# Kernel tuning notes

Hardware: AMD Instinct MI355X
Metric: run time of the kernel (lower is better)

The kernel has to match this reference:

```python
import jax, jax.numpy as jnp
import numpy as np

B, F, D, A = 1024, 33, 128, 128  # batch, num_fields, embed_dim, attn_size (A must equal gnn dim)

def setup_inputs() -> dict:
    key = jax.random.key(0)
    k1, k2, k3, k4 = jax.random.split(key, 4)
    gnn_feature = jax.random.normal(k1, (B, A), dtype=jnp.float32)
    x = jax.random.normal(k2, (B, F, D), dtype=jnp.float32)
    # attention Linear(embed_dim -> attn_size): weight (A, D), bias (A,)
    lim = 1.0 / np.sqrt(D)
    attn_W = jax.random.uniform(k3, (A, D), minval=-lim, maxval=lim, dtype=jnp.float32)
    attn_b = jax.random.uniform(k4, (A,), minval=-lim, maxval=lim, dtype=jnp.float32)
    return {"gnn_feature": gnn_feature, "x": x, "attn_W": attn_W, "attn_b": attn_b}

def reference(gnn_feature, x, attn_W, attn_b):
    num_fields = x.shape[1]
    row, col = np.triu_indices(num_fields, k=1)  # P = F*(F-1)/2 pairs
    inner = x[:, row] * x[:, col]                # [B, P, D]
    fm = jax.nn.relu(jnp.einsum('bpd,ad->bpa', inner, attn_W) + attn_b)  # [B, P, A]
    # bmm(gnn[b,1,A], fm[b,p,A,1]) -> dot product per pair, softmax over pairs
    scores = jnp.einsum('ba,bpa->bp', gnn_feature, fm)  # [B, P]
    attn = jax.nn.softmax(scores, axis=1)               # [B, P]
    attn_output = jnp.einsum('bp,bpd->bd', attn, inner) * 100.0  # [B, D]
    return jnp.concatenate([gnn_feature, attn_output], axis=1)   # [B, A+D]
```

## Files before the change

kernel.cpp:

```cpp
#include <hip/hip_runtime.h>

#define FN 33
#define DN 128
#define AN 128
#define PN 528
#define MTN 33
#define XS 136
#define AS 36

typedef __attribute__((ext_vector_type(8))) _Float16 half8;
typedef __attribute__((ext_vector_type(2))) _Float16 h2;
typedef __attribute__((ext_vector_type(4))) float f32x4;
typedef __attribute__((ext_vector_type(2))) float f32x2;
typedef __attribute__((ext_vector_type(4))) unsigned int u32x4;

__device__ __forceinline__ unsigned int pkrtz(float a, float b) {
  return __builtin_bit_cast(unsigned int, __builtin_amdgcn_cvt_pkrtz(a, b));
}
__device__ __forceinline__ h2 ash2(unsigned int u) { return __builtin_bit_cast(h2, u); }

__device__ __forceinline__ float row_sum16(float v) {
  v += __builtin_bit_cast(float, __builtin_amdgcn_update_dpp(0, __builtin_bit_cast(int, v), 0x128, 0xF, 0xF, false));
  v += __builtin_bit_cast(float, __builtin_amdgcn_update_dpp(0, __builtin_bit_cast(int, v), 0x124, 0xF, 0xF, false));
  v += __builtin_bit_cast(float, __builtin_amdgcn_update_dpp(0, __builtin_bit_cast(int, v), 0x122, 0xF, 0xF, false));
  v += __builtin_bit_cast(float, __builtin_amdgcn_update_dpp(0, __builtin_bit_cast(int, v), 0x121, 0xF, 0xF, false));
  return v;
}

__global__ __launch_bounds__(256, 2)
void afm_kernel(const float* __restrict__ gnn, const float* __restrict__ xg,
                const float* __restrict__ Wg,  const float* __restrict__ bg,
                float* __restrict__ out)
{
  __shared__ __align__(16) _Float16 xh[FN * XS];
  __shared__ __align__(16) unsigned int attn_h2[FN * AS];
  __shared__ __align__(16) float scores_s[PN];
  __shared__ __align__(16) float part[512];
  __shared__ unsigned short rowcol[PN];
  __shared__ float red[8];

  const int tid  = threadIdx.x;
  const int wave = tid >> 6;
  const int lane = tid & 63;
  const int q    = lane >> 4;
  const int u    = lane & 15;

  for (int p = tid; p < PN; p += 256) {
    int i = 0, rem = p;
    while (rem >= FN - 1 - i) { rem -= FN - 1 - i; i++; }
    rowcol[p] = (unsigned short)(i | ((i + 1 + rem) << 8));
  }
  half8 Bf[8][4];
  #pragma unroll
  for (int n = 0; n < 8; n++) {
    const float* wrow = Wg + (size_t)(n * 16 + u) * DN + q * 8;
    #pragma unroll
    for (int kk = 0; kk < 4; kk++) {
      f32x4 w0 = *(const f32x4*)(wrow + kk * 32);
      f32x4 w1 = *(const f32x4*)(wrow + kk * 32 + 4);
      union { half8 h; unsigned int w[4]; } t;
      t.w[0] = pkrtz(w0.x, w0.y);
      t.w[1] = pkrtz(w0.z, w0.w);
      t.w[2] = pkrtz(w1.x, w1.y);
      t.w[3] = pkrtz(w1.z, w1.w);
      Bf[n][kk] = t.h;
      asm volatile("" : "+v"(Bf[n][kk]));
    }
  }
  float barr[8];
  #pragma unroll
  for (int n = 0; n < 8; n++) { barr[n] = bg[n * 16 + u]; asm volatile("" : "+v"(barr[n])); }

  #pragma unroll 1
  for (int r2 = 0; r2 < 2; r2++) {
    const int b = blockIdx.x * 2 + r2;

    float garr[8];
    #pragma unroll
    for (int n = 0; n < 8; n++) { garr[n] = gnn[(size_t)b * AN + n * 16 + u]; asm volatile("" : "+v"(garr[n])); }

    const f32x4* xg4 = (const f32x4*)(xg + (size_t)b * FN * DN);
    for (int idx = tid; idx < (FN * DN) / 4; idx += 256) {
      f32x4 v = xg4[idx];
      int i  = idx >> 5;
      int d0 = (idx & 31) << 2;
      *(uint2*)&xh[i * XS + d0] = make_uint2(pkrtz(v.x, v.y), pkrtz(v.z, v.w));
    }
    for (int idx = tid; idx < FN * AS; idx += 256) attn_h2[idx] = 0u;
    __syncthreads();

    {
      int mt = wave;
      unsigned int rc = rowcol[mt * 16 + u];
      int r = rc & 255, c = rc >> 8;
      half8 xr[4], xc[4];
      #pragma unroll
      for (int kk = 0; kk < 4; kk++) {
        xr[kk] = *(const half8*)&xh[r * XS + kk * 32 + q * 8];
        xc[kk] = *(const half8*)&xh[c * XS + kk * 32 + q * 8];
      }
      for (;;) {
        half8 Af[4];
        #pragma unroll
        for (int kk = 0; kk < 4; kk++) Af[kk] = xr[kk] * xc[kk];

        const int nmt = mt + 4;
        if (nmt < MTN) {
          rc = rowcol[nmt * 16 + u];
          r = rc & 255; c = rc >> 8;
          #pragma unroll
          for (int kk = 0; kk < 4; kk++) {
            xr[kk] = *(const half8*)&xh[r * XS + kk * 32 + q * 8];
            xc[kk] = *(const half8*)&xh[c * XS + kk * 32 + q * 8];
          }
        }

        float sc[4] = {0.f, 0.f, 0.f, 0.f};
        #pragma unroll
        for (int g = 0; g < 2; g++) {
          f32x4 acc[4];
          #pragma unroll
          for (int nn = 0; nn < 4; nn++) {
            float bv = barr[g * 4 + nn];
            acc[nn] = (f32x4){bv, bv, bv, bv};
          }
          #pragma unroll
          for (int kk = 0; kk < 4; kk++)
            #pragma unroll
            for (int nn = 0; nn < 4; nn++)
              acc[nn] = __builtin_amdgcn_mfma_f32_16x16x32_f16(Af[kk], Bf[g * 4 + nn][kk], acc[nn], 0, 0, 0);
          #pragma unroll
          for (int nn = 0; nn < 4; nn++)
            #pragma unroll
            for (int rr = 0; rr < 4; rr++) {
              float fmv = fmaxf(acc[nn][rr], 0.f);
              sc[rr] = fmaf(fmv, garr[g * 4 + nn], sc[rr]);
            }
        }
        #pragma unroll
        for (int rr = 0; rr < 4; rr++) sc[rr] = row_sum16(sc[rr]);
        if (u == 0)
          *(f32x4*)&scores_s[mt * 16 + q * 4] = (f32x4){sc[0], sc[1], sc[2], sc[3]};

        if (nmt >= MTN) break;
        mt = nmt;
      }
    }
    __syncthreads();

    float s0 = scores_s[tid];
    float s1 = scores_s[tid + 256];
    float s2 = (tid < 16) ? scores_s[tid + 512] : -3.4e38f;
    float m = fmaxf(fmaxf(s0, s1), s2);
    #pragma unroll
    for (int off = 32; off >= 1; off >>= 1) m = fmaxf(m, __shfl_xor(m, off, 64));
    if (lane == 0) red[wave] = m;
    __syncthreads();
    const float smax = fmaxf(fmaxf(red[0], red[1]), fmaxf(red[2], red[3]));

    float e0 = __expf(s0 - smax);
    float e1 = __expf(s1 - smax);
    float e2 = (tid < 16) ? __expf(s2 - smax) : 0.f;
    {
      unsigned int rc = rowcol[tid];
      attn_h2[(rc & 255) * AS + ((rc >> 8) - (rc & 255) - 1)] = pkrtz(e0, e0);
      rc = rowcol[tid + 256];
      attn_h2[(rc & 255) * AS + ((rc >> 8) - (rc & 255) - 1)] = pkrtz(e1, e1);
      if (tid < 16) {
        rc = rowcol[tid + 512];
        attn_h2[(rc & 255) * AS + ((rc >> 8) - (rc & 255) - 1)] = pkrtz(e2, e2);
      }
    }
    float lsum = e0 + e1 + e2;
    #pragma unroll
    for (int off = 32; off >= 1; off >>= 1) lsum += __shfl_xor(lsum, off, 64);
    if (lane == 0) red[4 + wave] = lsum;
    __syncthreads();
    const float Z = red[4] + red[5] + red[6] + red[7];

    {
      unsigned int xp[36];
      #pragma unroll
      for (int j = 0; j < FN; j++) xp[j] = *(const unsigned int*)&xh[j * XS + 2 * lane];
      xp[33] = 0u; xp[34] = 0u; xp[35] = 0u;

      float a0 = 0.f, a1 = 0.f;
      #pragma unroll
      for (int i = 0; i < 32; i++) {
        if ((i & 3) != wave) continue;
        const int L   = 32 - i;
        const int n4  = (L + 3) >> 2;
        h2 ti2 = (h2)0.0f;
        #pragma unroll
        for (int t = 0; t < 8; t++) {
          if (t >= n4) break;
          u32x4 a4 = *(const u32x4*)&attn_h2[i * AS + 4 * t];
          ti2 += ash2(a4.x) * ash2(xp[i + 1 + 4 * t + 0]);
          ti2 += ash2(a4.y) * ash2(xp[i + 1 + 4 * t + 1]);
          ti2 += ash2(a4.z) * ash2(xp[i + 1 + 4 * t + 2]);
          ti2 += ash2(a4.w) * ash2(xp[i + 1 + 4 * t + 3]);
        }
        h2 xi = ash2(xp[i]);
        a0 = fmaf((float)xi[0], (float)ti2[0], a0);
        a1 = fmaf((float)xi[1], (float)ti2[1], a1);
      }
      *(f32x2*)&part[wave * 128 + 2 * lane] = (f32x2){a0, a1};
    }
    __syncthreads();
    if (tid < DN) {
      float tot = (part[tid] + part[128 + tid]) + (part[256 + tid] + part[384 + tid]);
      out[(size_t)b * (AN + DN) + AN + tid] = tot * (100.0f / Z);
    } else {
      const int a = tid - 128;
      out[(size_t)b * (AN + DN) + a] = gnn[(size_t)b * AN + a];
    }
  }
}

extern "C" void kernel_launch(void* const* d_in, const int* in_sizes, int n_in,
                              void* d_out, int out_size, void* d_ws, size_t ws_size,
                              hipStream_t stream) {
  (void)n_in; (void)out_size; (void)d_ws; (void)ws_size;
  const float* gnn  = (const float*)d_in[0];
  const float* x    = (const float*)d_in[1];
  const float* W    = (const float*)d_in[2];
  const float* bias = (const float*)d_in[3];
  float* out = (float*)d_out;
  const int Bn = in_sizes[0] / AN;
  afm_kernel<<<dim3(Bn / 2), dim3(256), 0, stream>>>(gnn, x, W, bias, out);
}
```

Before: 121.4 us.

## Use one 128-thread block per batch row instead of 256 threads per two rows

The kernel now launches one block of 2 waves for each batch element instead of 4 waves handling two batch elements in sequence. The x tile load and its fp16 conversion now start before the W fragment conversion, so that global latency overlaps with building the weight fragments. Each wave now processes more M-tiles and more pair rows, and the softmax reductions are sized for 2 waves. The intent is better latency hiding and more blocks in flight across CUs. The cost is that every block reloads and reconverts W, which doubles that per-block setup work.

```diff
diff --git a/kernel.cpp b/kernel.cpp
--- a/kernel.cpp
+++ b/kernel.cpp
@@ -27,7 +27,7 @@
   return v;
 }
 
-__global__ __launch_bounds__(256, 2)
+__global__ __launch_bounds__(128, 2)
 void afm_kernel(const float* __restrict__ gnn, const float* __restrict__ xg,
                 const float* __restrict__ Wg,  const float* __restrict__ bg,
                 float* __restrict__ out)
@@ -35,21 +35,31 @@
   __shared__ __align__(16) _Float16 xh[FN * XS];
   __shared__ __align__(16) unsigned int attn_h2[FN * AS];
   __shared__ __align__(16) float scores_s[PN];
-  __shared__ __align__(16) float part[512];
+  __shared__ __align__(16) float part[256];
   __shared__ unsigned short rowcol[PN];
-  __shared__ float red[8];
+  __shared__ float red[4];
 
   const int tid  = threadIdx.x;
+  const int b    = blockIdx.x;
   const int wave = tid >> 6;
   const int lane = tid & 63;
   const int q    = lane >> 4;
   const int u    = lane & 15;
 
-  for (int p = tid; p < PN; p += 256) {
+  for (int p = tid; p < PN; p += 128) {
     int i = 0, rem = p;
     while (rem >= FN - 1 - i) { rem -= FN - 1 - i; i++; }
     rowcol[p] = (unsigned short)(i | ((i + 1 + rem) << 8));
   }
+  const f32x4* xg4 = (const f32x4*)(xg + (size_t)b * FN * DN);
+  for (int idx = tid; idx < (FN * DN) / 4; idx += 128) {
+    f32x4 v = xg4[idx];
+    int i  = idx >> 5;
+    int d0 = (idx & 31) << 2;
+    *(uint2*)&xh[i * XS + d0] = make_uint2(pkrtz(v.x, v.y), pkrtz(v.z, v.w));
+  }
+  for (int idx = tid; idx < FN * AS; idx += 128) attn_h2[idx] = 0u;
+
   half8 Bf[8][4];
   #pragma unroll
   for (int n = 0; n < 8; n++) {
@@ -67,153 +77,144 @@
       asm volatile("" : "+v"(Bf[n][kk]));
     }
   }
-  float barr[8];
-  #pragma unroll
-  for (int n = 0; n < 8; n++) { barr[n] = bg[n * 16 + u]; asm volatile("" : "+v"(barr[n])); }
-
-  #pragma unroll 1
-  for (int r2 = 0; r2 < 2; r2++) {
-    const int b = blockIdx.x * 2 + r2;
-
-    float garr[8];
-    #pragma unroll
-    for (int n = 0; n < 8; n++) { garr[n] = gnn[(size_t)b * AN + n * 16 + u]; asm volatile("" : "+v"(garr[n])); }
-
-    const f32x4* xg4 = (const f32x4*)(xg + (size_t)b * FN * DN);
-    for (int idx = tid; idx < (FN * DN) / 4; idx += 256) {
-      f32x4 v = xg4[idx];
-      int i  = idx >> 5;
-      int d0 = (idx & 31) << 2;
-      *(uint2*)&xh[i * XS + d0] = make_uint2(pkrtz(v.x, v.y), pkrtz(v.z, v.w));
-    }
-    for (int idx = tid; idx < FN * AS; idx += 256) attn_h2[idx] = 0u;
-    __syncthreads();
-
-    {
-      int mt = wave;
-      unsigned int rc = rowcol[mt * 16 + u];
-      int r = rc & 255, c = rc >> 8;
-      half8 xr[4], xc[4];
-      #pragma unroll
-      for (int kk = 0; kk < 4; kk++) {
-        xr[kk] = *(const half8*)&xh[r * XS + kk * 32 + q * 8];
-        xc[kk] = *(const half8*)&xh[c * XS + kk * 32 + q * 8];
+  float barr[8], garr[8];
+  #pragma unroll
+  for (int n = 0; n < 8; n++) {
+    barr[n] = bg[n * 16 + u];
+    garr[n] = gnn[(size_t)b * AN + n * 16 + u];
+  }
+  __syncthreads();
+
+  {
+    int mt = wave;
+    unsigned int rc = rowcol[mt * 16 + u];
+    int r = rc & 255, c = rc >> 8;
+    half8 xr[4], xc[4];
+    #pragma unroll
+    for (int kk = 0; kk < 4; kk++) {
+      xr[kk] = *(const half8*)&xh[r * XS + kk * 32 + q * 8];
+      xc[kk] = *(const half8*)&xh[c * XS + kk * 32 + q * 8];
+    }
+    for (;;) {
+      half8 Af[4];
+      #pragma unroll
+      for (int kk = 0; kk < 4; kk++) Af[kk] = xr[kk] * xc[kk];
+
+      const int nmt = mt + 2;
+      if (nmt < MTN) {
+        rc = rowcol[nmt * 16 + u];
+        r = rc & 255; c = rc >> 8;
+        #pragma unroll
+        for (int kk = 0; kk < 4; kk++) {
+          xr[kk] = *(const half8*)&xh[r * XS + kk * 32 + q * 8];
+          xc[kk] = *(const half8*)&xh[c * XS + kk * 32 + q * 8];
+        }
       }
-      for (;;) {
-        half8 Af[4];
-        #pragma unroll
-        for (int kk = 0; kk < 4; kk++) Af[kk] = xr[kk] * xc[kk];
-
-        const int nmt = mt + 4;
-        if (nmt < MTN) {
-          rc = rowcol[nmt * 16 + u];
-          r = rc & 255; c = rc >> 8;
-          #pragma unroll
-          for (int kk = 0; kk < 4; kk++) {
-            xr[kk] = *(const half8*)&xh[r * XS + kk * 32 + q * 8];
-            xc[kk] = *(const half8*)&xh[c * XS + kk * 32 + q * 8];
-          }
+
+      float sc[4] = {0.f, 0.f, 0.f, 0.f};
+      #pragma unroll
+      for (int g = 0; g < 2; g++) {
+        f32x4 acc[4];
+        #pragma unroll
+        for (int nn = 0; nn < 4; nn++) {
+          float bv = barr[g * 4 + nn];
+          acc[nn] = (f32x4){bv, bv, bv, bv};
         }
-
-        float sc[4] = {0.f, 0.f, 0.f, 0.f};
-        #pragma unroll
-        for (int g = 0; g < 2; g++) {
-          f32x4 acc[4];
-          #pragma unroll
-          for (int nn = 0; nn < 4; nn++) {
-            float bv = barr[g * 4 + nn];
-            acc[nn] = (f32x4){bv, bv, bv, bv};
-          }
-          #pragma unroll
-          for (int kk = 0; kk < 4; kk++)
-            #pragma unroll
-            for (int nn = 0; nn < 4; nn++)
-              acc[nn] = __builtin_amdgcn_mfma_f32_16x16x32_f16(Af[kk], Bf[g * 4 + nn][kk], acc[nn], 0, 0, 0);
+        #pragma unroll
+        for (int kk = 0; kk < 4; kk++)
           #pragma unroll
           for (int nn = 0; nn < 4; nn++)
-            #pragma unroll
-            for (int rr = 0; rr < 4; rr++) {
-              float fmv = fmaxf(acc[nn][rr], 0.f);
-              sc[rr] = fmaf(fmv, garr[g * 4 + nn], sc[rr]);
-            }
-        }
-        #pragma unroll
-        for (int rr = 0; rr < 4; rr++) sc[rr] = row_sum16(sc[rr]);
-        if (u == 0)
-          *(f32x4*)&scores_s[mt * 16 + q * 4] = (f32x4){sc[0], sc[1], sc[2], sc[3]};
-
-        if (nmt >= MTN) break;
-        mt = nmt;
+            acc[nn] = __builtin_amdgcn_mfma_f32_16x16x32_f16(Af[kk], Bf[g * 4 + nn][kk], acc[nn], 0, 0, 0);
+        #pragma unroll
+        for (int nn = 0; nn < 4; nn++)
+          #pragma unroll
+          for (int rr = 0; rr < 4; rr++) {
+            float fmv = fmaxf(acc[nn][rr], 0.f);
+            sc[rr] = fmaf(fmv, garr[g * 4 + nn], sc[rr]);
+          }
       }
-    }
-    __syncthreads();
-
-    float s0 = scores_s[tid];
-    float s1 = scores_s[tid + 256];
-    float s2 = (tid < 16) ? scores_s[tid + 512] : -3.4e38f;
-    float m = fmaxf(fmaxf(s0, s1), s2);
-    #pragma unroll
-    for (int off = 32; off >= 1; off >>= 1) m = fmaxf(m, __shfl_xor(m, off, 64));
-    if (lane == 0) red[wave] = m;
-    __syncthreads();
-    const float smax = fmaxf(fmaxf(red[0], red[1]), fmaxf(red[2], red[3]));
-
-    float e0 = __expf(s0 - smax);
-    float e1 = __expf(s1 - smax);
-    float e2 = (tid < 16) ? __expf(s2 - smax) : 0.f;
-    {
-      unsigned int rc = rowcol[tid];
-      attn_h2[(rc & 255) * AS + ((rc >> 8) - (rc & 255) - 1)] = pkrtz(e0, e0);
-      rc = rowcol[tid + 256];
-      attn_h2[(rc & 255) * AS + ((rc >> 8) - (rc & 255) - 1)] = pkrtz(e1, e1);
-      if (tid < 16) {
-        rc = rowcol[tid + 512];
-        attn_h2[(rc & 255) * AS + ((rc >> 8) - (rc & 255) - 1)] = pkrtz(e2, e2);
+      #pragma unroll
+      for (int rr = 0; rr < 4; rr++) sc[rr] = row_sum16(sc[rr]);
+      if (u == 0)
+        *(f32x4*)&scores_s[mt * 16 + q * 4] = (f32x4){sc[0], sc[1], sc[2], sc[3]};
+
+      if (nmt >= MTN) break;
+      mt = nmt;
+    }
+  }
+  __syncthreads();
+
+  float s0 = scores_s[tid];
+  float s1 = scores_s[tid + 128];
+  float s2 = scores_s[tid + 256];
+  float s3 = scores_s[tid + 384];
+  float s4 = (tid < 16) ? scores_s[tid + 512] : -3.4e38f;
+  float m = fmaxf(fmaxf(fmaxf(s0, s1), fmaxf(s2, s3)), s4);
+  #pragma unroll
+  for (int off = 32; off >= 1; off >>= 1) m = fmaxf(m, __shfl_xor(m, off, 64));
+  if (lane == 0) red[wave] = m;
+  __syncthreads();
+  const float smax = fmaxf(red[0], red[1]);
+
+  float e0 = __expf(s0 - smax);
+  float e1 = __expf(s1 - smax);
+  float e2 = __expf(s2 - smax);
+  float e3 = __expf(s3 - smax);
+  float e4 = (tid < 16) ? __expf(s4 - smax) : 0.f;
+  {
+    unsigned int rc = rowcol[tid];
+    attn_h2[(rc & 255) * AS + ((rc >> 8) - (rc & 255) - 1)] = pkrtz(e0, e0);
+    rc = rowcol[tid + 128];
+    attn_h2[(rc & 255) * AS + ((rc >> 8) - (rc & 255) - 1)] = pkrtz(e1, e1);
+    rc = rowcol[tid + 256];
+    attn_h2[(rc & 255) * AS + ((rc >> 8) - (rc & 255) - 1)] = pkrtz(e2, e2);
+    rc = rowcol[tid + 384];
+    attn_h2[(rc & 255) * AS + ((rc >> 8) - (rc & 255) - 1)] = pkrtz(e3, e3);
+    if (tid < 16) {
+      rc = rowcol[tid + 512];
+      attn_h2[(rc & 255) * AS + ((rc >> 8) - (rc & 255) - 1)] = pkrtz(e4, e4);
+    }
+  }
+  float lsum = (e0 + e1) + (e2 + e3) + e4;
+  #pragma unroll
+  for (int off = 32; off >= 1; off >>= 1) lsum += __shfl_xor(lsum, off, 64);
+  if (lane == 0) red[2 + wave] = lsum;
+  __syncthreads();
+  const float Z = red[2] + red[3];
+
+  {
+    unsigned int xp[36];
+    #pragma unroll
+    for (int j = 0; j < FN; j++) xp[j] = *(const unsigned int*)&xh[j * XS + 2 * lane];
+    xp[33] = 0u; xp[34] = 0u; xp[35] = 0u;
+
+    float a0 = 0.f, a1 = 0.f;
+    #pragma unroll
+    for (int i = 0; i < 32; i++) {
+      if ((i & 1) != wave) continue;
+      const int L  = 32 - i;
+      const int n4 = (L + 3) >> 2;
+      h2 ti2 = (h2)0.0f;
+      #pragma unroll
+      for (int t = 0; t < 8; t++) {
+        if (t >= n4) break;
+        u32x4 a4 = *(const u32x4*)&attn_h2[i * AS + 4 * t];
+        ti2 += ash2(a4.x) * ash2(xp[i + 1 + 4 * t + 0]);
+        ti2 += ash2(a4.y) * ash2(xp[i + 1 + 4 * t + 1]);
+        ti2 += ash2(a4.z) * ash2(xp[i + 1 + 4 * t + 2]);
+        ti2 += ash2(a4.w) * ash2(xp[i + 1 + 4 * t + 3]);
       }
-    }
-    float lsum = e0 + e1 + e2;
-    #pragma unroll
-    for (int off = 32; off >= 1; off >>= 1) lsum += __shfl_xor(lsum, off, 64);
-    if (lane == 0) red[4 + wave] = lsum;
-    __syncthreads();
-    const float Z = red[4] + red[5] + red[6] + red[7];
-
-    {
-      unsigned int xp[36];
-      #pragma unroll
-      for (int j = 0; j < FN; j++) xp[j] = *(const unsigned int*)&xh[j * XS + 2 * lane];
-      xp[33] = 0u; xp[34] = 0u; xp[35] = 0u;
-
-      float a0 = 0.f, a1 = 0.f;
-      #pragma unroll
-      for (int i = 0; i < 32; i++) {
-        if ((i & 3) != wave) continue;
-        const int L   = 32 - i;
-        const int n4  = (L + 3) >> 2;
-        h2 ti2 = (h2)0.0f;
-        #pragma unroll
-        for (int t = 0; t < 8; t++) {
-          if (t >= n4) break;
-          u32x4 a4 = *(const u32x4*)&attn_h2[i * AS + 4 * t];
-          ti2 += ash2(a4.x) * ash2(xp[i + 1 + 4 * t + 0]);
-          ti2 += ash2(a4.y) * ash2(xp[i + 1 + 4 * t + 1]);
-          ti2 += ash2(a4.z) * ash2(xp[i + 1 + 4 * t + 2]);
-          ti2 += ash2(a4.w) * ash2(xp[i + 1 + 4 * t + 3]);
-        }
-        h2 xi = ash2(xp[i]);
-        a0 = fmaf((float)xi[0], (float)ti2[0], a0);
-        a1 = fmaf((float)xi[1], (float)ti2[1], a1);
-      }
-      *(f32x2*)&part[wave * 128 + 2 * lane] = (f32x2){a0, a1};
-    }
-    __syncthreads();
-    if (tid < DN) {
-      float tot = (part[tid] + part[128 + tid]) + (part[256 + tid] + part[384 + tid]);
-      out[(size_t)b * (AN + DN) + AN + tid] = tot * (100.0f / Z);
-    } else {
-      const int a = tid - 128;
-      out[(size_t)b * (AN + DN) + a] = gnn[(size_t)b * AN + a];
-    }
+      h2 xi = ash2(xp[i]);
+      a0 = fmaf((float)xi[0], (float)ti2[0], a0);
+      a1 = fmaf((float)xi[1], (float)ti2[1], a1);
+    }
+    *(f32x2*)&part[wave * 128 + 2 * lane] = (f32x2){a0, a1};
+  }
+  __syncthreads();
+  {
+    out[(size_t)b * (AN + DN) + tid] = gnn[(size_t)b * AN + tid];
+    float tot = part[tid] + part[128 + tid];
+    out[(size_t)b * (AN + DN) + AN + tid] = tot * (100.0f / Z);
   }
 }
 
@@ -227,5 +228,5 @@
   const float* bias = (const float*)d_in[3];
   float* out = (float*)d_out;
   const int Bn = in_sizes[0] / AN;
-  afm_kernel<<<dim3(Bn / 2), dim3(256), 0, stream>>>(gnn, x, W, bias, out);
-}
+  afm_kernel<<<dim3(Bn), dim3(128), 0, stream>>>(gnn, x, W, bias, out);
+}
```

New measurement: 110.1 us. 1.1x faster.

## Split MFMA work across M/N wave halves, one batch row per block

Applied to the files above, without the earlier changes.

Each block now handles a single batch row instead of two, so the grid doubles. The four waves are split into two M-halves and two N-halves, so each wave holds only half of the W fragments. This lowers register pressure enough to raise the occupancy hint to 3 blocks per CU. Partial scores from the two N-halves are summed in shared memory, and every wave computes the softmax max and sum redundantly, which removes the cross-wave reduction barriers. The cost is that W is converted and loaded per block twice as often, and each pair tile's A operand is built by two waves.

```diff
diff --git a/kernel.cpp b/kernel.cpp
--- a/kernel.cpp
+++ b/kernel.cpp
@@ -7,6 +7,7 @@
 #define MTN 33
 #define XS 136
 #define AS 36
+#define SS 544
 
 typedef __attribute__((ext_vector_type(8))) _Float16 half8;
 typedef __attribute__((ext_vector_type(2))) _Float16 h2;
@@ -27,33 +28,44 @@
   return v;
 }
 
-__global__ __launch_bounds__(256, 2)
+__global__ __launch_bounds__(256, 3)
 void afm_kernel(const float* __restrict__ gnn, const float* __restrict__ xg,
                 const float* __restrict__ Wg,  const float* __restrict__ bg,
                 float* __restrict__ out)
 {
   __shared__ __align__(16) _Float16 xh[FN * XS];
   __shared__ __align__(16) unsigned int attn_h2[FN * AS];
-  __shared__ __align__(16) float scores_s[PN];
+  __shared__ __align__(16) float scores2[2 * SS];
   __shared__ __align__(16) float part[512];
   __shared__ unsigned short rowcol[PN];
-  __shared__ float red[8];
 
   const int tid  = threadIdx.x;
+  const int b    = blockIdx.x;
   const int wave = tid >> 6;
   const int lane = tid & 63;
   const int q    = lane >> 4;
   const int u    = lane & 15;
+  const int mh   = wave >> 1;
+  const int nh   = wave & 1;
 
   for (int p = tid; p < PN; p += 256) {
     int i = 0, rem = p;
     while (rem >= FN - 1 - i) { rem -= FN - 1 - i; i++; }
     rowcol[p] = (unsigned short)(i | ((i + 1 + rem) << 8));
   }
-  half8 Bf[8][4];
-  #pragma unroll
-  for (int n = 0; n < 8; n++) {
-    const float* wrow = Wg + (size_t)(n * 16 + u) * DN + q * 8;
+  const f32x4* xg4 = (const f32x4*)(xg + (size_t)b * FN * DN);
+  for (int idx = tid; idx < (FN * DN) / 4; idx += 256) {
+    f32x4 v = xg4[idx];
+    int i  = idx >> 5;
+    int d0 = (idx & 31) << 2;
+    *(uint2*)&xh[i * XS + d0] = make_uint2(pkrtz(v.x, v.y), pkrtz(v.z, v.w));
+  }
+  for (int idx = tid; idx < FN * AS; idx += 256) attn_h2[idx] = 0u;
+
+  half8 Bf[4][4];
+  #pragma unroll
+  for (int nn = 0; nn < 4; nn++) {
+    const float* wrow = Wg + (size_t)((nh * 4 + nn) * 16 + u) * DN + q * 8;
     #pragma unroll
     for (int kk = 0; kk < 4; kk++) {
       f32x4 w0 = *(const f32x4*)(wrow + kk * 32);
@@ -63,157 +75,138 @@
       t.w[1] = pkrtz(w0.z, w0.w);
       t.w[2] = pkrtz(w1.x, w1.y);
       t.w[3] = pkrtz(w1.z, w1.w);
-      Bf[n][kk] = t.h;
-      asm volatile("" : "+v"(Bf[n][kk]));
-    }
-  }
-  float barr[8];
-  #pragma unroll
-  for (int n = 0; n < 8; n++) { barr[n] = bg[n * 16 + u]; asm volatile("" : "+v"(barr[n])); }
-
-  #pragma unroll 1
-  for (int r2 = 0; r2 < 2; r2++) {
-    const int b = blockIdx.x * 2 + r2;
-
-    float garr[8];
-    #pragma unroll
-    for (int n = 0; n < 8; n++) { garr[n] = gnn[(size_t)b * AN + n * 16 + u]; asm volatile("" : "+v"(garr[n])); }
-
-    const f32x4* xg4 = (const f32x4*)(xg + (size_t)b * FN * DN);
-    for (int idx = tid; idx < (FN * DN) / 4; idx += 256) {
-      f32x4 v = xg4[idx];
-      int i  = idx >> 5;
-      int d0 = (idx & 31) << 2;
-      *(uint2*)&xh[i * XS + d0] = make_uint2(pkrtz(v.x, v.y), pkrtz(v.z, v.w));
-    }
-    for (int idx = tid; idx < FN * AS; idx += 256) attn_h2[idx] = 0u;
-    __syncthreads();
-
-    {
-      int mt = wave;
-      unsigned int rc = rowcol[mt * 16 + u];
-      int r = rc & 255, c = rc >> 8;
-      half8 xr[4], xc[4];
+      Bf[nn][kk] = t.h;
+      asm volatile("" : "+v"(Bf[nn][kk]));
+    }
+  }
+  float garr[4];
+  f32x4 bias_acc[4];
+  #pragma unroll
+  for (int nn = 0; nn < 4; nn++) {
+    const int a = (nh * 4 + nn) * 16 + u;
+    garr[nn] = gnn[(size_t)b * AN + a];
+    float bv = bg[a];
+    bias_acc[nn] = (f32x4){bv, bv, bv, bv};
+    asm volatile("" : "+v"(garr[nn]), "+v"(bias_acc[nn]));
+  }
+  __syncthreads();
+
+  {
+    int mt = mh;
+    unsigned int rc = rowcol[mt * 16 + u];
+    int r = rc & 255, c = rc >> 8;
+    half8 xr[4], xc[4];
+    #pragma unroll
+    for (int kk = 0; kk < 4; kk++) {
+      xr[kk] = *(const half8*)&xh[r * XS + kk * 32 + q * 8];
+      xc[kk] = *(const half8*)&xh[c * XS + kk * 32 + q * 8];
+    }
+    for (;;) {
+      f32x4 acc[4];
       #pragma unroll
       for (int kk = 0; kk < 4; kk++) {
-        xr[kk] = *(const half8*)&xh[r * XS + kk * 32 + q * 8];
-        xc[kk] = *(const half8*)&xh[c * XS + kk * 32 + q * 8];
+        half8 Af = xr[kk] * xc[kk];
+        #pragma unroll
+        for (int nn = 0; nn < 4; nn++)
+          acc[nn] = __builtin_amdgcn_mfma_f32_16x16x32_f16(
+              Af, Bf[nn][kk], kk == 0 ? bias_acc[nn] : acc[nn], 0, 0, 0);
       }
-      for (;;) {
-        half8 Af[4];
+
+      const int nmt = mt + 2;
+      if (nmt < MTN) {
+        rc = rowcol[nmt * 16 + u];
+        r = rc & 255; c = rc >> 8;
         #pragma unroll
-        for (int kk = 0; kk < 4; kk++) Af[kk] = xr[kk] * xc[kk];
-
-        const int nmt = mt + 4;
-        if (nmt < MTN) {
-          rc = rowcol[nmt * 16 + u];
-          r = rc & 255; c = rc >> 8;
-          #pragma unroll
-          for (int kk = 0; kk < 4; kk++) {
-            xr[kk] = *(const half8*)&xh[r * XS + kk * 32 + q * 8];
-            xc[kk] = *(const half8*)&xh[c * XS + kk * 32 + q * 8];
-          }
+        for (int kk = 0; kk < 4; kk++) {
+          xr[kk] = *(const half8*)&xh[r * XS + kk * 32 + q * 8];
+          xc[kk] = *(const half8*)&xh[c * XS + kk * 32 + q * 8];
         }
-
-        float sc[4] = {0.f, 0.f, 0.f, 0.f};
+      }
+
+      float sc[4] = {0.f, 0.f, 0.f, 0.f};
+      #pragma unroll
+      for (int nn = 0; nn < 4; nn++)
         #pragma unroll
-        for (int g = 0; g < 2; g++) {
-          f32x4 acc[4];
-          #pragma unroll
-          for (int nn = 0; nn < 4; nn++) {
-            float bv = barr[g * 4 + nn];
-            acc[nn] = (f32x4){bv, bv, bv, bv};
-          }
-          #pragma unroll
-          for (int kk = 0; kk < 4; kk++)
-            #pragma unroll
-            for (int nn = 0; nn < 4; nn++)
-              acc[nn] = __builtin_amdgcn_mfma_f32_16x16x32_f16(Af[kk], Bf[g * 4 + nn][kk], acc[nn], 0, 0, 0);
-          #pragma unroll
-          for (int nn = 0; nn < 4; nn++)
-            #pragma unroll
-            for (int rr = 0; rr < 4; rr++) {
-              float fmv = fmaxf(acc[nn][rr], 0.f);
-              sc[rr] = fmaf(fmv, garr[g * 4 + nn], sc[rr]);
-            }
+        for (int rr = 0; rr < 4; rr++) {
+          float fmv = fmaxf(acc[nn][rr], 0.f);
+          sc[rr] = fmaf(fmv, garr[nn], sc[rr]);
         }
-        #pragma unroll
-        for (int rr = 0; rr < 4; rr++) sc[rr] = row_sum16(sc[rr]);
-        if (u == 0)
-          *(f32x4*)&scores_s[mt * 16 + q * 4] = (f32x4){sc[0], sc[1], sc[2], sc[3]};
-
-        if (nmt >= MTN) break;
-        mt = nmt;
+      #pragma unroll
+      for (int rr = 0; rr < 4; rr++) sc[rr] = row_sum16(sc[rr]);
+      if (u == 0)
+        *(f32x4*)&scores2[nh * SS + mt * 16 + q * 4] = (f32x4){sc[0], sc[1], sc[2], sc[3]};
+
+      if (nmt >= MTN) break;
+      mt = nmt;
+    }
+  }
+  __syncthreads();
+
+  float s[9], e[9];
+  #pragma unroll
+  for (int t = 0; t < 8; t++)
+    s[t] = scores2[t * 64 + lane] + scores2[SS + t * 64 + lane];
+  s[8] = (lane < 16) ? (scores2[512 + lane] + scores2[SS + 512 + lane]) : -3.4e38f;
+  float m = s[0];
+  #pragma unroll
+  for (int t = 1; t < 9; t++) m = fmaxf(m, s[t]);
+  #pragma unroll
+  for (int off = 32; off >= 1; off >>= 1) m = fmaxf(m, __shfl_xor(m, off, 64));
+  float lsum = 0.f;
+  #pragma unroll
+  for (int t = 0; t < 9; t++) {
+    e[t] = (t == 8 && lane >= 16) ? 0.f : __expf(s[t] - m);
+    lsum += e[t];
+  }
+  #pragma unroll
+  for (int off = 32; off >= 1; off >>= 1) lsum += __shfl_xor(lsum, off, 64);
+  const float Z = lsum;
+
+  #pragma unroll
+  for (int t = 0; t < 9; t++) {
+    bool mine = (t < 8) ? ((t >> 1) == wave) : (wave == 3 && lane < 16);
+    if (mine) {
+      unsigned int rc = rowcol[t * 64 + lane];
+      attn_h2[(rc & 255) * AS + ((rc >> 8) - (rc & 255) - 1)] = pkrtz(e[t], e[t]);
+    }
+  }
+  __syncthreads();
+
+  {
+    unsigned int xp[36];
+    #pragma unroll
+    for (int j = 0; j < FN; j++) xp[j] = *(const unsigned int*)&xh[j * XS + 2 * lane];
+    xp[33] = 0u; xp[34] = 0u; xp[35] = 0u;
+
+    float a0 = 0.f, a1 = 0.f;
+    #pragma unroll
+    for (int i = 0; i < 32; i++) {
+      if ((i & 3) != wave) continue;
+      const int L  = 32 - i;
+      const int n4 = (L + 3) >> 2;
+      h2 ti2 = (h2)0.0f;
+      #pragma unroll
+      for (int t = 0; t < 8; t++) {
+        if (t >= n4) break;
+        u32x4 a4 = *(const u32x4*)&attn_h2[i * AS + 4 * t];
+        ti2 += ash2(a4.x) * ash2(xp[i + 1 + 4 * t + 0]);
+        ti2 += ash2(a4.y) * ash2(xp[i + 1 + 4 * t + 1]);
+        ti2 += ash2(a4.z) * ash2(xp[i + 1 + 4 * t + 2]);
+        ti2 += ash2(a4.w) * ash2(xp[i + 1 + 4 * t + 3]);
       }
-    }
-    __syncthreads();
-
-    float s0 = scores_s[tid];
-    float s1 = scores_s[tid + 256];
-    float s2 = (tid < 16) ? scores_s[tid + 512] : -3.4e38f;
-    float m = fmaxf(fmaxf(s0, s1), s2);
-    #pragma unroll
-    for (int off = 32; off >= 1; off >>= 1) m = fmaxf(m, __shfl_xor(m, off, 64));
-    if (lane == 0) red[wave] = m;
-    __syncthreads();
-    const float smax = fmaxf(fmaxf(red[0], red[1]), fmaxf(red[2], red[3]));
-
-    float e0 = __expf(s0 - smax);
-    float e1 = __expf(s1 - smax);
-    float e2 = (tid < 16) ? __expf(s2 - smax) : 0.f;
-    {
-      unsigned int rc = rowcol[tid];
-      attn_h2[(rc & 255) * AS + ((rc >> 8) - (rc & 255) - 1)] = pkrtz(e0, e0);
-      rc = rowcol[tid + 256];
-      attn_h2[(rc & 255) * AS + ((rc >> 8) - (rc & 255) - 1)] = pkrtz(e1, e1);
-      if (tid < 16) {
-        rc = rowcol[tid + 512];
-        attn_h2[(rc & 255) * AS + ((rc >> 8) - (rc & 255) - 1)] = pkrtz(e2, e2);
-      }
-    }
-    float lsum = e0 + e1 + e2;
-    #pragma unroll
-    for (int off = 32; off >= 1; off >>= 1) lsum += __shfl_xor(lsum, off, 64);
-    if (lane == 0) red[4 + wave] = lsum;
-    __syncthreads();
-    const float Z = red[4] + red[5] + red[6] + red[7];
-
-    {
-      unsigned int xp[36];
-      #pragma unroll
-      for (int j = 0; j < FN; j++) xp[j] = *(const unsigned int*)&xh[j * XS + 2 * lane];
-      xp[33] = 0u; xp[34] = 0u; xp[35] = 0u;
-
-      float a0 = 0.f, a1 = 0.f;
-      #pragma unroll
-      for (int i = 0; i < 32; i++) {
-        if ((i & 3) != wave) continue;
-        const int L   = 32 - i;
-        const int n4  = (L + 3) >> 2;
-        h2 ti2 = (h2)0.0f;
-        #pragma unroll
-        for (int t = 0; t < 8; t++) {
-          if (t >= n4) break;
-          u32x4 a4 = *(const u32x4*)&attn_h2[i * AS + 4 * t];
-          ti2 += ash2(a4.x) * ash2(xp[i + 1 + 4 * t + 0]);
-          ti2 += ash2(a4.y) * ash2(xp[i + 1 + 4 * t + 1]);
-          ti2 += ash2(a4.z) * ash2(xp[i + 1 + 4 * t + 2]);
-          ti2 += ash2(a4.w) * ash2(xp[i + 1 + 4 * t + 3]);
-        }
-        h2 xi = ash2(xp[i]);
-        a0 = fmaf((float)xi[0], (float)ti2[0], a0);
-        a1 = fmaf((float)xi[1], (float)ti2[1], a1);
-      }
-      *(f32x2*)&part[wave * 128 + 2 * lane] = (f32x2){a0, a1};
-    }
-    __syncthreads();
-    if (tid < DN) {
-      float tot = (part[tid] + part[128 + tid]) + (part[256 + tid] + part[384 + tid]);
-      out[(size_t)b * (AN + DN) + AN + tid] = tot * (100.0f / Z);
-    } else {
-      const int a = tid - 128;
-      out[(size_t)b * (AN + DN) + a] = gnn[(size_t)b * AN + a];
-    }
+      h2 xi = ash2(xp[i]);
+      a0 = fmaf((float)xi[0], (float)ti2[0], a0);
+      a1 = fmaf((float)xi[1], (float)ti2[1], a1);
+    }
+    *(f32x2*)&part[wave * 128 + 2 * lane] = (f32x2){a0, a1};
+  }
+  __syncthreads();
+  if (tid < DN) {
+    float tot = (part[tid] + part[128 + tid]) + (part[256 + tid] + part[384 + tid]);
+    out[(size_t)b * (AN + DN) + AN + tid] = tot * (100.0f / Z);
+  } else {
+    const int a = tid - 128;
+    out[(size_t)b * (AN + DN) + a] = gnn[(size_t)b * AN + a];
   }
 }
 
@@ -227,5 +220,5 @@
   const float* bias = (const float*)d_in[3];
   float* out = (float*)d_out;
   const int Bn = in_sizes[0] / AN;
-  afm_kernel<<<dim3(Bn / 2), dim3(256), 0, stream>>>(gnn, x, W, bias, out);
-}
+  afm_kernel<<<dim3(Bn), dim3(256), 0, stream>>>(gnn, x, W, bias, out);
+}
```

Result: faster. 109.6 us (-9.8%).
